# Kernel optimization log

Measured on AMD Instinct MI355X. Metric: run time of the kernel, lower is better.

The kernel has to match this reference:

```python
import jax, jax.numpy as jnp
import numpy as np

NUM_HEADS = 8
LN_EPS = 1e-5


def _layer_norm(x, g, b):
    mu = jnp.mean(x, axis=-1, keepdims=True)
    var = jnp.mean(jnp.square(x - mu), axis=-1, keepdims=True)
    return (x - mu) * jax.lax.rsqrt(var + LN_EPS) * g + b


def setup_inputs() -> dict:
    key = jax.random.key(0)
    ks = jax.random.split(key, 8)
    B, N, D = 8, 2048, 256
    s = 0.02
    return {
        "x": jax.random.normal(ks[0], (B, N, D), jnp.float32),
        "pos": jax.random.normal(ks[1], (B, N, 2 * D), jnp.float32),
        "mask": jax.random.randint(ks[2], (B, N), 0, 2) > 0,  # True = padded key
        "Wqkv": jax.random.normal(ks[3], (D, 3 * D), jnp.float32) * s,
        "bqkv": jnp.zeros((3 * D,), jnp.float32),
        "Wpos": jax.random.normal(ks[4], (2 * D, 2 * D), jnp.float32) * s,
        "bpos": jnp.zeros((2 * D,), jnp.float32),
        "ln1_g": jnp.ones((D,), jnp.float32),
        "ln1_b": jnp.zeros((D,), jnp.float32),
        "W1": jax.random.normal(ks[5], (D, 4 * D), jnp.float32) * s,
        "b1": jnp.zeros((4 * D,), jnp.float32),
        "W2": jax.random.normal(ks[6], (4 * D, D), jnp.float32) * s,
        "b2": jnp.zeros((D,), jnp.float32),
        "ln2_g": jnp.ones((D,), jnp.float32),
        "ln2_b": jnp.zeros((D,), jnp.float32),
    }


def reference(x, pos, mask, Wqkv, bqkv, Wpos, bpos, ln1_g, ln1_b,
              W1, b1, W2, b2, ln2_g, ln2_b):
    B, N, D = x.shape
    H = NUM_HEADS
    Dh = D // H

    qkv = x @ Wqkv + bqkv                      # [B,N,3D]
    q, k, v = jnp.split(qkv, 3, axis=-1)       # each [B,N,D]
    qk_pos = pos @ Wpos + bpos                 # [B,N,2D]
    q_pos, k_pos = jnp.split(qk_pos, 2, axis=-1)
    q = q + q_pos
    k = k + k_pos

    # [B,N,D] -> [B,H,N,Dh]
    q = q.reshape(B, N, H, Dh).transpose(0, 2, 1, 3)
    k = k.reshape(B, N, H, Dh).transpose(0, 2, 1, 3)
    v = v.reshape(B, N, H, Dh).transpose(0, 2, 1, 3)

    scores = jnp.einsum('bhqd,bhkd->bhqk', q, k) / jnp.sqrt(jnp.float32(Dh))
    scores = jnp.where(mask[:, None, None, :], -jnp.inf, scores)
    attn = jax.nn.softmax(scores, axis=-1)
    out = jnp.einsum('bhqk,bhkd->bhqd', attn, v)
    out = out.transpose(0, 2, 1, 3).reshape(B, N, D)

    h = _layer_norm(x + out, ln1_g, ln1_b)
    ffn = jax.nn.relu(h @ W1 + b1) @ W2 + b2
    return _layer_norm(h + ffn, ln2_g, ln2_b)
```

## Files before the change

kernel.cpp:

```cpp
#include <hip/hip_runtime.h>
#include <math.h>

#define BATCH 8
#define SEQ   2048
#define DIM   256
#define NHEAD 8
#define DHEAD 32
#define MROWS (BATCH*SEQ)
#define KCAT  768

typedef short bf16x8 __attribute__((ext_vector_type(8)));
typedef float f32x4  __attribute__((ext_vector_type(4)));
typedef float f32x16 __attribute__((ext_vector_type(16)));

#define CLSCALE 0.25503485f

static __device__ __forceinline__ float exp2_raw(float x) {
    float r;
    asm("v_exp_f32 %0, %1" : "=v"(r) : "v"(x));
    return r;
}

static __device__ __forceinline__ unsigned bf16rne(float f) {
    unsigned u = __float_as_uint(f);
    return (u + 0x7FFFu + ((u >> 16) & 1u)) >> 16;
}

__global__ __launch_bounds__(256) void convcat_kernel(
    const float* __restrict__ x, const float* __restrict__ pos,
    unsigned short* __restrict__ acat, int n1, int n2)
{
    int i = blockIdx.x * 256 + threadIdx.x;
    const float* s; size_t dst; int j;
    if (i < n1) {
        j = i; s = x;
        int row = j >> 5, c8 = (j & 31) * 8;
        dst = (size_t)row * KCAT + c8;
    } else {
        j = i - n1; if (j >= n2) return; s = pos;
        int row = j >> 6, c8 = (j & 63) * 8;
        dst = (size_t)row * KCAT + 256 + c8;
    }
    float4 a = ((const float4*)s)[2 * j];
    float4 b = ((const float4*)s)[2 * j + 1];
    union { unsigned short u[8]; uint4 v; } o;
    o.u[0] = bf16rne(a.x); o.u[1] = bf16rne(a.y);
    o.u[2] = bf16rne(a.z); o.u[3] = bf16rne(a.w);
    o.u[4] = bf16rne(b.x); o.u[5] = bf16rne(b.y);
    o.u[6] = bf16rne(b.z); o.u[7] = bf16rne(b.w);
    *(uint4*)&acat[dst] = o.v;
}

__global__ __launch_bounds__(256) void wtrans_all_kernel(
    const float* __restrict__ Wqkv, const float* __restrict__ Wpos,
    const float* __restrict__ W1, const float* __restrict__ W2,
    unsigned short* __restrict__ wqk, unsigned short* __restrict__ wv,
    unsigned short* __restrict__ w1, unsigned short* __restrict__ w2)
{
    int b = blockIdx.x;
    const float* src; unsigned short* dst;
    int srcN, srcColOff, dstK, dstKOff, nbx;
    if (b < 128)      {          src = Wqkv; dst = wqk; srcN = 768;  srcColOff = 0;   dstK = 768;  dstKOff = 0;   nbx = 16; }
    else if (b < 384) { b -= 128; src = Wpos; dst = wqk; srcN = 512;  srcColOff = 0;   dstK = 768;  dstKOff = 256; nbx = 16; }
    else if (b < 448) { b -= 384; src = Wqkv; dst = wv;  srcN = 768;  srcColOff = 512; dstK = 256;  dstKOff = 0;   nbx = 8;  }
    else if (b < 704) { b -= 448; src = W1;   dst = w1;  srcN = 1024; srcColOff = 0;   dstK = 256;  dstKOff = 0;   nbx = 32; }
    else              { b -= 704; src = W2;   dst = w2;  srcN = 256;  srcColOff = 0;   dstK = 1024; dstKOff = 0;   nbx = 8;  }
    const int tn0 = (b % nbx) * 32;
    const int tk0 = (b / nbx) * 32;

    __shared__ float tile[32][33];
    const int tx = threadIdx.x & 31;
    const int ty = threadIdx.x >> 5;
    #pragma unroll
    for (int r = ty; r < 32; r += 8)
        tile[r][tx] = src[(size_t)(tk0 + r) * srcN + srcColOff + tn0 + tx];
    __syncthreads();
    #pragma unroll
    for (int r = ty; r < 32; r += 8)
        dst[(size_t)(tn0 + r) * dstK + dstKOff + tk0 + tx] =
            (unsigned short)bf16rne(tile[tx][r]);
}

template<int MODE>
static __device__ __forceinline__ void mgemm_body(
    int bx, int by,
    const unsigned short* __restrict__ A, const unsigned short* __restrict__ Wt,
    const float* __restrict__ bias, const float* __restrict__ bias2,
    float* __restrict__ C, unsigned short* __restrict__ Cb,
    int M, int K, int Nc, int lda,
    unsigned short* __restrict__ u0, unsigned short* __restrict__ u1,
    unsigned short* __restrict__ u2)
{
    const int t    = threadIdx.x;
    const int wv   = t >> 6;
    const int lane = t & 63;
    const int g    = lane >> 4;
    const int lo   = lane & 15;
    const int wr   = wv >> 1;
    const int wc   = wv & 1;
    const int r0   = by * 128 + wr * 64;
    const int c0   = bx * 128 + wc * 64;

    f32x4 acc[4][4];
    #pragma unroll
    for (int i = 0; i < 4; ++i)
        #pragma unroll
        for (int j = 0; j < 4; ++j)
            #pragma unroll
            for (int r = 0; r < 4; ++r) acc[i][j][r] = 0.f;

    const unsigned short* aP[4];
    const unsigned short* bP[4];
    #pragma unroll
    for (int i = 0; i < 4; ++i) {
        aP[i] = A  + (size_t)(r0 + 16 * i + lo) * lda + g * 8;
        bP[i] = Wt + (size_t)(c0 + 16 * i + lo) * K + g * 8;
    }

    bf16x8 aA[4], bA[4], aB[4], bB[4];
    #pragma unroll
    for (int i = 0; i < 4; ++i) {
        aA[i] = *(const bf16x8*)(aP[i]);
        bA[i] = *(const bf16x8*)(bP[i]);
    }

    for (int k0 = 0; k0 < K; k0 += 64) {
        #pragma unroll
        for (int i = 0; i < 4; ++i) {
            aB[i] = *(const bf16x8*)(aP[i] + k0 + 32);
            bB[i] = *(const bf16x8*)(bP[i] + k0 + 32);
        }
        #pragma unroll
        for (int i = 0; i < 4; ++i)
            #pragma unroll
            for (int j = 0; j < 4; ++j)
                acc[i][j] = __builtin_amdgcn_mfma_f32_16x16x32_bf16(
                    aA[i], bA[j], acc[i][j], 0, 0, 0);
        if (k0 + 64 < K) {
            #pragma unroll
            for (int i = 0; i < 4; ++i) {
                aA[i] = *(const bf16x8*)(aP[i] + k0 + 64);
                bA[i] = *(const bf16x8*)(bP[i] + k0 + 64);
            }
        }
        #pragma unroll
        for (int i = 0; i < 4; ++i)
            #pragma unroll
            for (int j = 0; j < 4; ++j)
                acc[i][j] = __builtin_amdgcn_mfma_f32_16x16x32_bf16(
                    aB[i], bB[j], acc[i][j], 0, 0, 0);
    }

    #pragma unroll
    for (int j = 0; j < 4; ++j) {
        const int col = c0 + 16 * j + lo;
        const float bs = bias[col] + ((MODE == 4) ? bias2[col] : 0.f);
        #pragma unroll
        for (int i = 0; i < 4; ++i) {
            if (MODE == 5) {
                const int row0 = r0 + 16 * i + g * 4;
                const int bb   = row0 >> 11;
                const int nn0  = row0 & (SEQ - 1);
                const int hh   = col >> 5;
                const int dh   = col & 31;
                uint2 pk;
                pk.x = bf16rne(acc[i][j][0] + bs) | (bf16rne(acc[i][j][1] + bs) << 16);
                pk.y = bf16rne(acc[i][j][2] + bs) | (bf16rne(acc[i][j][3] + bs) << 16);
                *(uint2*)&u2[(((size_t)bb * NHEAD + hh) * DHEAD + dh) * SEQ + nn0] = pk;
            } else {
                #pragma unroll
                for (int r = 0; r < 4; ++r) {
                    const int row = r0 + 16 * i + g * 4 + r;
                    float v = acc[i][j][r] + bs;
                    if (MODE == 0) {
                        C[(size_t)row * Nc + col] = v;
                    } else if (MODE == 1) {
                        Cb[(size_t)row * Nc + col] =
                            (unsigned short)bf16rne(fmaxf(v, 0.f));
                    } else {
                        const int bb = row >> 11;
                        const int nn = row & (SEQ - 1);
                        const int which = col >> 8;
                        const int d  = col & 255;
                        const int hh = d >> 5;
                        const int dh = d & 31;
                        const size_t dst =
                            (((size_t)bb * NHEAD + hh) * SEQ + nn) * DHEAD + dh;
                        if (which == 0) {
                            u0[dst] = (unsigned short)bf16rne(v * CLSCALE);
                        } else {
                            u1[dst] = (unsigned short)bf16rne(v);
                        }
                    }
                }
            }
        }
    }
}

template<int MODE>
__global__ __launch_bounds__(256, 3) void mgemm_kernel(
    const unsigned short* __restrict__ A, const unsigned short* __restrict__ Wt,
    const float* __restrict__ bias, const float* __restrict__ bias2,
    float* __restrict__ C, unsigned short* __restrict__ Cb,
    int M, int K, int Nc, int lda,
    unsigned short* __restrict__ u0, unsigned short* __restrict__ u1,
    unsigned short* __restrict__ u2)
{
    mgemm_body<MODE>(blockIdx.x, blockIdx.y, A, Wt, bias, bias2, C, Cb,
                     M, K, Nc, lda, u0, u1, u2);
}

__global__ __launch_bounds__(256, 3) void qkv_kernel(
    const unsigned short* __restrict__ acat,
    const unsigned short* __restrict__ wqk, const unsigned short* __restrict__ wv,
    const float* __restrict__ bqkv, const float* __restrict__ bpos,
    unsigned short* __restrict__ qb, unsigned short* __restrict__ kb,
    unsigned short* __restrict__ vt)
{
    const int b = blockIdx.x;
    if (b < 512) {
        mgemm_body<4>(b & 3, b >> 2, acat, wqk, bqkv, bpos, nullptr, nullptr,
                      MROWS, KCAT, 512, KCAT, qb, kb, nullptr);
    } else {
        const int b2 = b - 512;
        mgemm_body<5>(b2 & 1, b2 >> 1, acat, wv, bqkv + 512, nullptr,
                      nullptr, nullptr, MROWS, 256, 256, KCAT,
                      nullptr, nullptr, vt);
    }
}

__global__ __launch_bounds__(256) void attn_kernel(
    const unsigned short* __restrict__ Qb, const unsigned short* __restrict__ Kb,
    const unsigned short* __restrict__ Vt, const int* __restrict__ mask,
    float* __restrict__ O)
{
    __shared__ float bias_s[SEQ];

    const int t    = threadIdx.x;
    const int wv   = t >> 6;
    const int lane = t & 63;
    const int h    = lane >> 5;
    const int ql   = lane & 31;

    const int sb   = ((blockIdx.x & 7) << 6) | (blockIdx.x >> 3);
    const int bh   = sb >> 3;
    const int qblk = sb & 7;
    const int bb   = bh >> 3;
    const int hh   = bh & 7;
    const int qt   = qblk * 256 + wv * 64;

    const int* mrow = mask + bb * SEQ;
    for (int i = t; i < SEQ; i += 256)
        bias_s[i] = mrow[i] ? -3.0e38f : 0.0f;
    __syncthreads();

    const unsigned short* Qh = Qb + (size_t)bh * SEQ * 32;
    const unsigned short* Kh = Kb + (size_t)bh * SEQ * 32;
    const unsigned short* Vh = Vt + (size_t)bh * 32 * SEQ;

    bf16x8 qf[2][2];
    #pragma unroll
    for (int i = 0; i < 2; ++i)
        #pragma unroll
        for (int dh = 0; dh < 2; ++dh)
            qf[i][dh] = *(const bf16x8*)&Qh[(size_t)(qt + 32 * i + ql) * 32 + 16 * dh + 8 * h];

    f32x16 acc[2];
    #pragma unroll
    for (int i = 0; i < 2; ++i)
        #pragma unroll
        for (int r = 0; r < 16; ++r) acc[i][r] = 0.f;
    float l[2] = {0.f, 0.f};

    for (int k0 = 0; k0 < SEQ; k0 += 32) {
        bf16x8 kf0 = *(const bf16x8*)&Kh[(size_t)(k0 + ql) * 32 + 8 * h];
        bf16x8 kf1 = *(const bf16x8*)&Kh[(size_t)(k0 + ql) * 32 + 16 + 8 * h];
        bf16x8 vf0 = *(const bf16x8*)&Vh[(size_t)ql * SEQ + k0 + 8 * h];
        bf16x8 vf1 = *(const bf16x8*)&Vh[(size_t)ql * SEQ + k0 + 16 + 8 * h];

        f32x16 cbv;
        #pragma unroll
        for (int c = 0; c < 4; ++c) {
            f32x4 cb = *(const f32x4*)&bias_s[k0 + 4 * h + 8 * c];
            #pragma unroll
            for (int e = 0; e < 4; ++e) cbv[4 * c + e] = cb[e];
        }

        #pragma unroll
        for (int i = 0; i < 2; ++i) {
            __builtin_amdgcn_s_setprio(1);
            f32x16 s = __builtin_amdgcn_mfma_f32_32x32x16_bf16(
                kf0, qf[i][0], cbv, 0, 0, 0);
            s = __builtin_amdgcn_mfma_f32_32x32x16_bf16(
                kf1, qf[i][1], s, 0, 0, 0);
            __builtin_amdgcn_s_setprio(0);

            float p[16];
            float tl = 0.f;
            #pragma unroll
            for (int r = 0; r < 16; ++r) {
                p[r] = exp2_raw(s[r]);
                tl += p[r];
            }
            l[i] += tl;

            unsigned w00, w01, w10, w11, w20, w21, w30, w31;
            asm("v_cvt_pk_bf16_f32 %0, %1, %2" : "=v"(w00) : "v"(p[0]),  "v"(p[1]));
            asm("v_cvt_pk_bf16_f32 %0, %1, %2" : "=v"(w01) : "v"(p[2]),  "v"(p[3]));
            asm("v_cvt_pk_bf16_f32 %0, %1, %2" : "=v"(w10) : "v"(p[4]),  "v"(p[5]));
            asm("v_cvt_pk_bf16_f32 %0, %1, %2" : "=v"(w11) : "v"(p[6]),  "v"(p[7]));
            asm("v_cvt_pk_bf16_f32 %0, %1, %2" : "=v"(w20) : "v"(p[8]),  "v"(p[9]));
            asm("v_cvt_pk_bf16_f32 %0, %1, %2" : "=v"(w21) : "v"(p[10]), "v"(p[11]));
            asm("v_cvt_pk_bf16_f32 %0, %1, %2" : "=v"(w30) : "v"(p[12]), "v"(p[13]));
            asm("v_cvt_pk_bf16_f32 %0, %1, %2" : "=v"(w31) : "v"(p[14]), "v"(p[15]));
            asm volatile("v_permlane32_swap_b32 %0, %1" : "+v"(w00), "+v"(w10));
            asm volatile("v_permlane32_swap_b32 %0, %1" : "+v"(w01), "+v"(w11));
            asm volatile("v_permlane32_swap_b32 %0, %1" : "+v"(w20), "+v"(w30));
            asm volatile("v_permlane32_swap_b32 %0, %1" : "+v"(w21), "+v"(w31));
            union { unsigned u[4]; bf16x8 v; } pa, pb;
            pa.u[0] = w00; pa.u[1] = w01; pa.u[2] = w10; pa.u[3] = w11;
            pb.u[0] = w20; pb.u[1] = w21; pb.u[2] = w30; pb.u[3] = w31;

            __builtin_amdgcn_s_setprio(1);
            acc[i] = __builtin_amdgcn_mfma_f32_32x32x16_bf16(
                vf0, pa.v, acc[i], 0, 0, 0);
            acc[i] = __builtin_amdgcn_mfma_f32_32x32x16_bf16(
                vf1, pb.v, acc[i], 0, 0, 0);
            __builtin_amdgcn_s_setprio(0);
        }
    }

    #pragma unroll
    for (int i = 0; i < 2; ++i) {
        l[i] += __shfl_xor(l[i], 32);
        const float inv = (l[i] > 0.f) ? 1.0f / l[i] : 0.f;
        const size_t rowoff = (size_t)(bb * SEQ + qt + 32 * i + ql) * DIM + hh * 32;
        #pragma unroll
        for (int c = 0; c < 4; ++c) {
            float4 ov;
            ov.x = acc[i][4 * c + 0] * inv;
            ov.y = acc[i][4 * c + 1] * inv;
            ov.z = acc[i][4 * c + 2] * inv;
            ov.w = acc[i][4 * c + 3] * inv;
            *(float4*)&O[rowoff + 4 * h + 8 * c] = ov;
        }
    }
}

__global__ __launch_bounds__(256) void ln_kernel(
    const float* __restrict__ X, const float* __restrict__ R,
    const float* __restrict__ gam, const float* __restrict__ bet,
    float* __restrict__ Y, unsigned short* __restrict__ Yb)
{
    const int lane = threadIdx.x & 63;
    const int row  = blockIdx.x * 4 + (threadIdx.x >> 6);
    const size_t off = (size_t)row * DIM + lane * 4;

    float4 xv = *(const float4*)&X[off];
    float4 rv = *(const float4*)&R[off];
    float4 v;
    v.x = xv.x + rv.x; v.y = xv.y + rv.y;
    v.z = xv.z + rv.z; v.w = xv.w + rv.w;

    float s = (v.x + v.y) + (v.z + v.w);
    #pragma unroll
    for (int o = 1; o < 64; o <<= 1) s += __shfl_xor(s, o);
    const float mu = s * (1.f / 256.f);

    float4 d;
    d.x = v.x - mu; d.y = v.y - mu; d.z = v.z - mu; d.w = v.w - mu;
    float s2 = (d.x * d.x + d.y * d.y) + (d.z * d.z + d.w * d.w);
    #pragma unroll
    for (int o = 1; o < 64; o <<= 1) s2 += __shfl_xor(s2, o);
    const float rs = rsqrtf(s2 * (1.f / 256.f) + 1e-5f);

    float4 gv = *(const float4*)&gam[lane * 4];
    float4 bv = *(const float4*)&bet[lane * 4];
    float4 y;
    y.x = d.x * rs * gv.x + bv.x;
    y.y = d.y * rs * gv.y + bv.y;
    y.z = d.z * rs * gv.z + bv.z;
    y.w = d.w * rs * gv.w + bv.w;
    *(float4*)&Y[off] = y;

    if (Yb) {
        uint2 pk;
        pk.x = bf16rne(y.x) | (bf16rne(y.y) << 16);
        pk.y = bf16rne(y.z) | (bf16rne(y.w) << 16);
        *(uint2*)&Yb[off] = pk;
    }
}

extern "C" void kernel_launch(void* const* d_in, const int* in_sizes, int n_in,
                              void* d_out, int out_size, void* d_ws, size_t ws_size,
                              hipStream_t stream)
{
    const float* x    = (const float*)d_in[0];
    const float* pos  = (const float*)d_in[1];
    const int*   mask = (const int*)d_in[2];
    const float* Wqkv = (const float*)d_in[3];
    const float* bqkv = (const float*)d_in[4];
    const float* Wpos = (const float*)d_in[5];
    const float* bpos = (const float*)d_in[6];
    const float* ln1g = (const float*)d_in[7];
    const float* ln1b = (const float*)d_in[8];
    const float* W1   = (const float*)d_in[9];
    const float* b1   = (const float*)d_in[10];
    const float* W2   = (const float*)d_in[11];
    const float* b2   = (const float*)d_in[12];
    const float* ln2g = (const float*)d_in[13];
    const float* ln2b = (const float*)d_in[14];
    float* out = (float*)d_out;

    char* base = (char*)d_ws;
    const size_t MB = 1024 * 1024;
    const size_t SZ = (size_t)MROWS * DIM;
    unsigned short* acat = (unsigned short*)(base + 0);
    float*          ao   = (float*)(base + 0);
    unsigned short* mid  = (unsigned short*)(base + 0);
    unsigned short* qb   = (unsigned short*)(base + 34 * MB);
    unsigned short* kb   = (unsigned short*)(base + 42 * MB);
    unsigned short* vt   = (unsigned short*)(base + 58 * MB);
    unsigned short* hb   = (unsigned short*)(base + 66 * MB);
    float*          hbuf = (float*)(base + 74 * MB);
    unsigned short* wqk  = (unsigned short*)(base + 90 * MB);
    unsigned short* wv   = wqk + 512 * 768;
    unsigned short* w1   = wv + 256 * 256;
    unsigned short* w2   = w1 + 1024 * 256;
    float*          f2   = out;

    dim3 blk(256);

    convcat_kernel<<<dim3((3 * (int)(SZ / 8)) / 256), blk, 0, stream>>>(
        x, pos, acat, (int)(SZ / 8), (int)(2 * SZ / 8));
    wtrans_all_kernel<<<dim3(960), blk, 0, stream>>>(
        Wqkv, Wpos, W1, W2, wqk, wv, w1, w2);
    qkv_kernel<<<dim3(768), blk, 0, stream>>>(
        acat, wqk, wv, bqkv, bpos, qb, kb, vt);
    attn_kernel<<<dim3(BATCH * NHEAD * (SEQ / 256)), blk, 0, stream>>>(
        qb, kb, vt, mask, ao);
    ln_kernel<<<dim3(MROWS / 4), blk, 0, stream>>>(x, ao, ln1g, ln1b, hbuf, hb);
    mgemm_kernel<1><<<dim3(1024 / 128, MROWS / 128), blk, 0, stream>>>(
        hb, w1, b1, nullptr, nullptr, mid, MROWS, 256, 1024, 256,
        nullptr, nullptr, nullptr);
    mgemm_kernel<0><<<dim3(256 / 128, MROWS / 128), blk, 0, stream>>>(
        mid, w2, b2, nullptr, f2, nullptr, MROWS, 1024, 256, 1024,
        nullptr, nullptr, nullptr);
    ln_kernel<<<dim3(MROWS / 4), blk, 0, stream>>>(hbuf, f2, ln2g, ln2b, out, nullptr);
}
```

Baseline: 238.1 us.

## Add dedicated FFN2 GEMM kernel with smaller tiles and direct register loads

Replaces the generic mgemm kernel for the second FFN matmul (K=1024, N=256) with a specialized kernel. It uses 64x128 block tiles instead of 128x128, which doubles the block count to improve occupancy on a narrow output. Operands are loaded straight from global memory into registers with double-buffered prefetch, and no LDS staging is used. This costs redundant global and L2 traffic, since tiles are no longer shared through shared memory, and the output stores are uncoalesced.

After: 246.9 us. 3.7% more time.

```diff
diff --git a/kernel.cpp b/kernel.cpp
--- a/kernel.cpp
+++ b/kernel.cpp
@@ -230,6 +230,84 @@
     }
 }
 
+__global__ __launch_bounds__(256, 3) void ffn2_kernel(
+    const unsigned short* __restrict__ A, const unsigned short* __restrict__ Wt,
+    const float* __restrict__ bias, float* __restrict__ C)
+{
+    const int K  = 1024;
+    const int Nc = 256;
+    const int t    = threadIdx.x;
+    const int wv   = t >> 6;
+    const int lane = t & 63;
+    const int g    = lane >> 4;
+    const int lo   = lane & 15;
+    const int wr   = wv >> 1;
+    const int wc   = wv & 1;
+    const int r0   = blockIdx.y * 64 + wr * 32;
+    const int c0   = blockIdx.x * 128 + wc * 64;
+
+    f32x4 acc[2][4];
+    #pragma unroll
+    for (int i = 0; i < 2; ++i)
+        #pragma unroll
+        for (int j = 0; j < 4; ++j)
+            #pragma unroll
+            for (int r = 0; r < 4; ++r) acc[i][j][r] = 0.f;
+
+    const unsigned short* aP[2];
+    const unsigned short* bP[4];
+    #pragma unroll
+    for (int i = 0; i < 2; ++i)
+        aP[i] = A  + (size_t)(r0 + 16 * i + lo) * K + g * 8;
+    #pragma unroll
+    for (int j = 0; j < 4; ++j)
+        bP[j] = Wt + (size_t)(c0 + 16 * j + lo) * K + g * 8;
+
+    bf16x8 aA[2], bA[4], aB[2], bB[4];
+    #pragma unroll
+    for (int i = 0; i < 2; ++i) aA[i] = *(const bf16x8*)(aP[i]);
+    #pragma unroll
+    for (int j = 0; j < 4; ++j) bA[j] = *(const bf16x8*)(bP[j]);
+
+    for (int k0 = 0; k0 < K; k0 += 64) {
+        #pragma unroll
+        for (int i = 0; i < 2; ++i) aB[i] = *(const bf16x8*)(aP[i] + k0 + 32);
+        #pragma unroll
+        for (int j = 0; j < 4; ++j) bB[j] = *(const bf16x8*)(bP[j] + k0 + 32);
+        #pragma unroll
+        for (int i = 0; i < 2; ++i)
+            #pragma unroll
+            for (int j = 0; j < 4; ++j)
+                acc[i][j] = __builtin_amdgcn_mfma_f32_16x16x32_bf16(
+                    aA[i], bA[j], acc[i][j], 0, 0, 0);
+        if (k0 + 64 < K) {
+            #pragma unroll
+            for (int i = 0; i < 2; ++i) aA[i] = *(const bf16x8*)(aP[i] + k0 + 64);
+            #pragma unroll
+            for (int j = 0; j < 4; ++j) bA[j] = *(const bf16x8*)(bP[j] + k0 + 64);
+        }
+        #pragma unroll
+        for (int i = 0; i < 2; ++i)
+            #pragma unroll
+            for (int j = 0; j < 4; ++j)
+                acc[i][j] = __builtin_amdgcn_mfma_f32_16x16x32_bf16(
+                    aB[i], bB[j], acc[i][j], 0, 0, 0);
+    }
+
+    #pragma unroll
+    for (int j = 0; j < 4; ++j) {
+        const int col = c0 + 16 * j + lo;
+        const float bs = bias[col];
+        #pragma unroll
+        for (int i = 0; i < 2; ++i)
+            #pragma unroll
+            for (int r = 0; r < 4; ++r) {
+                const int row = r0 + 16 * i + g * 4 + r;
+                C[(size_t)row * Nc + col] = acc[i][j][r] + bs;
+            }
+    }
+}
+
 __global__ __launch_bounds__(256) void attn_kernel(
     const unsigned short* __restrict__ Qb, const unsigned short* __restrict__ Kb,
     const unsigned short* __restrict__ Vt, const int* __restrict__ mask,
@@ -444,8 +522,7 @@
     mgemm_kernel<1><<<dim3(1024 / 128, MROWS / 128), blk, 0, stream>>>(
         hb, w1, b1, nullptr, nullptr, mid, MROWS, 256, 1024, 256,
         nullptr, nullptr, nullptr);
-    mgemm_kernel<0><<<dim3(256 / 128, MROWS / 128), blk, 0, stream>>>(
-        mid, w2, b2, nullptr, f2, nullptr, MROWS, 1024, 256, 1024,
-        nullptr, nullptr, nullptr);
+    ffn2_kernel<<<dim3(256 / 128, MROWS / 64), blk, 0, stream>>>(
+        mid, w2, b2, f2);
     ln_kernel<<<dim3(MROWS / 4), blk, 0, stream>>>(hbuf, f2, ln2g, ln2b, out, nullptr);
 }
```
